# Kernel optimization log

Hardware: AMD Instinct MI355X
Metric: run time of the kernel (lower is better)

Reference implementation:

```python
import jax, jax.numpy as jnp
import numpy as np

EPS = 1e-5
BT_BATCH = 32       # BarlowTwinsLoss init batch_size (divides c)
BT_LAMBD = 0.005

def seg_sum(v, idx, n):
    return jax.ops.segment_sum(v, idx, num_segments=n)

def seg_mean(v, idx, n):
    s = seg_sum(v, idx, n)
    c = seg_sum(jnp.ones((v.shape[0],), v.dtype), idx, n)
    return s / jnp.maximum(c, 1.0)[:, None]

def gcn_conv(x, W, b, edge_index):
    n = x.shape[0]
    src, dst = edge_index[0], edge_index[1]
    xw = x @ W
    deg = 1.0 + seg_sum(jnp.ones(src.shape, x.dtype), dst, n)  # self-loop included
    norm = jax.lax.rsqrt(deg[src] * deg[dst])
    out = seg_sum(norm[:, None] * xw[src], dst, n) + xw / deg[:, None]
    return out + b

def barlow(z1, z2):
    # z-score with unbiased std (torch.std), then BatchNorm1d(affine=False) stats
    def std1(z):
        return (z - z.mean(0)) / jnp.std(z, axis=0, ddof=1)
    def bn(z):
        return (z - z.mean(0)) / jnp.sqrt(z.var(0) + EPS)
    a, b = bn(std1(z1)), bn(std1(z2))
    c = (a.T @ b) / BT_BATCH
    d = jnp.diagonal(c)
    on_diag = jnp.sum((d - 1.0) ** 2)
    off_diag = jnp.sum(c ** 2) - jnp.sum(d ** 2)
    return on_diag + BT_LAMBD * off_diag

def layernorm(t, g, b):
    m = t.mean(-1, keepdims=True)
    v = t.var(-1, keepdims=True)
    return g * (t - m) / jnp.sqrt(v + EPS) + b

def setup_inputs() -> dict:
    key = jax.random.key(0)
    ks = jax.random.split(key, 24)
    N, M, d, B = 50000, 10000, 128, 32
    NNZ, EG, EE = 200000, 600000, 160000
    s = 1.0 / np.sqrt(d)
    inp = {
        'x': jax.random.normal(ks[0], (N, d), jnp.float32),
        'hyperedge_feature': jax.random.normal(ks[1], (M, d), jnp.float32),
        'node_coord': jax.random.normal(ks[2], (N, 3), jnp.float32),
        'hyperedge_node_idx': jax.random.randint(ks[3], (NNZ,), 0, N),
        'hyperedge_edge_idx': jax.random.randint(ks[4], (NNZ,), 0, M),
        'node_batch_idx': jnp.sort(jax.random.randint(ks[5], (N,), 0, B)),
        'hyperedge_batch_idx': jnp.sort(jax.random.randint(ks[6], (M,), 0, B)),
        'X_X': jax.random.randint(ks[7], (2, EG), 0, N),
        'E_E': jax.random.randint(ks[8], (2, EE), 0, M),
        'num_graphs': B,
        'Wv': jax.random.normal(ks[9], (d, d), jnp.float32) * s,
        'bv': jnp.zeros((d,), jnp.float32),
        'We': jax.random.normal(ks[10], (d, d), jnp.float32) * s,
        'be': jnp.zeros((d,), jnp.float32),
        'Wx': jax.random.normal(ks[11], (d, d), jnp.float32) * s,
        'bx': jnp.zeros((d,), jnp.float32),
        'Weg': jax.random.normal(ks[12], (d, d), jnp.float32) * s,
        'beg': jnp.zeros((d,), jnp.float32),
        'ln_g': jnp.ones((d,), jnp.float32),
        'ln_b': jnp.zeros((d,), jnp.float32),
        'Wf': jax.random.normal(ks[13], (2 * d, d), jnp.float32) * (1.0 / np.sqrt(2 * d)),
        'bf': jnp.zeros((d,), jnp.float32),
    }
    return inp

def reference(x, hyperedge_feature, node_coord, hyperedge_node_idx, hyperedge_edge_idx,
              node_batch_idx, hyperedge_batch_idx, X_X, E_E, num_graphs,
              Wv, bv, We, be, Wx, bx, Weg, beg, ln_g, ln_b, Wf, bf):
    N, d = x.shape
    M = hyperedge_feature.shape[0]
    ni, ei = hyperedge_node_idx, hyperedge_edge_idx
    # E_HypergraphConv: node<->hyperedge bipartite message passing + EGNN-style coord update
    xw = x @ Wv + bv                     # [N, d]
    ew = hyperedge_feature @ We + be     # [M, d]
    e_conv = seg_mean(xw[ni], ei, M)     # hyperedge update from member nodes
    z_conv = seg_mean(ew[ei], ni, N)     # node update from incident hyperedges
    edge_coord = seg_mean(node_coord[ni], ei, M)          # [M, 3]
    rel = node_coord[ni] - edge_coord[ei]                 # [nnz, 3]
    phi = jnp.tanh(jnp.sum(xw[ni] * ew[ei], -1, keepdims=True)
                   * jax.lax.rsqrt(jnp.asarray(float(d), x.dtype)))
    update_coord = node_coord + seg_mean(rel * phi, ni, N)
    # implicit graph branches
    z_imp = gcn_conv(x, Wx, bx, X_X)
    e_imp = gcn_conv(hyperedge_feature, Weg, beg, E_E)
    bt_loss = barlow(z_imp, z_conv) + barlow(e_imp, e_conv)
    # norm -> GELU (erf, torch default) -> dropout(eval=identity) -> residual
    z = jax.nn.gelu(layernorm(z_conv, ln_g, ln_b), approximate=False) + x
    e = jax.nn.gelu(layernorm(e_conv, ln_g, ln_b), approximate=False) + hyperedge_feature
    z_graph = seg_mean(z, node_batch_idx, num_graphs)
    e_graph = seg_mean(e, hyperedge_batch_idx, num_graphs)
    graph = jnp.concatenate([z_graph, e_graph], axis=1) @ Wf + bf
    return z, e, update_coord, graph, bt_loss
```

## Files before the change

### kernel.cpp

```cpp
#include <hip/hip_runtime.h>
#include <hip/hip_bf16.h>

#define NB 32
#define GPN 448
#define GPM 80
#define RGRP 16

__device__ __forceinline__ float wave_sum(float v) {
#pragma unroll
  for (int off = 32; off; off >>= 1) v += __shfl_xor(v, off);
  return v;
}
__device__ __forceinline__ int wave_sum_i(int v) {
#pragma unroll
  for (int off = 32; off; off >>= 1) v += __shfl_xor(v, off);
  return v;
}

__device__ __forceinline__ float bf2f(unsigned short u) {
  return __uint_as_float(((unsigned int)u) << 16);
}
__device__ __forceinline__ unsigned short f2bf(float f) {
  unsigned int v = __float_as_uint(f);
  return (unsigned short)((v + 0x7FFFu + ((v >> 16) & 1u)) >> 16);
}

__device__ __forceinline__ void gemm_body(const float* __restrict__ X,
                                          const float* __restrict__ W1,
                                          const float* __restrict__ b1,
                                          unsigned short* __restrict__ out1,
                                          const float* __restrict__ W2,
                                          unsigned short* __restrict__ out2, int rows,
                                          int blk, unsigned short (*xs)[132]) {
  const int t = threadIdx.x;
  const int c4 = t & 31;
  const int rg = t >> 5;
  const int r0 = blk * 64;
#pragma unroll
  for (int i = 0; i < 8; i++) {
    const int idx = t + i * 256;
    const int row = idx >> 5, cc = idx & 31;
    const int gr = r0 + row;
    float4 v = make_float4(0.f, 0.f, 0.f, 0.f);
    if (gr < rows) v = ((const float4*)X)[(size_t)gr * 32 + cc];
    ushort4 u;
    u.x = f2bf(v.x); u.y = f2bf(v.y); u.z = f2bf(v.z); u.w = f2bf(v.w);
    *(ushort4*)&xs[row][cc * 4] = u;
  }
  __syncthreads();
  const float4* W1v = (const float4*)W1;
  const float4* W2v = (const float4*)W2;
  const float4 b4 = ((const float4*)b1)[c4];
  float4 acc1[8], acc2[8];
#pragma unroll
  for (int i = 0; i < 8; i++) {
    acc1[i] = b4;
    acc2[i] = make_float4(0.f, 0.f, 0.f, 0.f);
  }
  const int rbase = rg * 8;
#pragma unroll 2
  for (int k = 0; k < 128; k++) {
    const float4 w1 = W1v[k * 32 + c4];
    const float4 w2 = W2v[k * 32 + c4];
#pragma unroll
    for (int i = 0; i < 8; i++) {
      const float xv = bf2f(xs[rbase + i][k]);
      acc1[i].x = fmaf(xv, w1.x, acc1[i].x);
      acc1[i].y = fmaf(xv, w1.y, acc1[i].y);
      acc1[i].z = fmaf(xv, w1.z, acc1[i].z);
      acc1[i].w = fmaf(xv, w1.w, acc1[i].w);
      acc2[i].x = fmaf(xv, w2.x, acc2[i].x);
      acc2[i].y = fmaf(xv, w2.y, acc2[i].y);
      acc2[i].z = fmaf(xv, w2.z, acc2[i].z);
      acc2[i].w = fmaf(xv, w2.w, acc2[i].w);
    }
  }
#pragma unroll
  for (int i = 0; i < 8; i++) {
    const int gr = r0 + rbase + i;
    if (gr < rows) {
      ushort4 o1, o2;
      o1.x = f2bf(acc1[i].x); o1.y = f2bf(acc1[i].y);
      o1.z = f2bf(acc1[i].z); o1.w = f2bf(acc1[i].w);
      o2.x = f2bf(acc2[i].x); o2.y = f2bf(acc2[i].y);
      o2.z = f2bf(acc2[i].z); o2.w = f2bf(acc2[i].w);
      ((ushort4*)out1)[(size_t)gr * 32 + c4] = o1;
      ((ushort4*)out2)[(size_t)gr * 32 + c4] = o2;
    }
  }
}

__global__ __launch_bounds__(256) void fused_stage1(
    const float* __restrict__ x, const float* __restrict__ Wv,
    const float* __restrict__ bv, unsigned short* __restrict__ xw,
    const float* __restrict__ Wx, unsigned short* __restrict__ xw2, int N, int nbGN,
    const float* __restrict__ hf, const float* __restrict__ We,
    const float* __restrict__ be, unsigned short* __restrict__ ew,
    const float* __restrict__ Weg, unsigned short* __restrict__ ew2, int M, int nbG,
    int nbCnt, int mn, const int* __restrict__ ni, const int* __restrict__ ei,
    int nnz, const int* __restrict__ xx, int eg, const int* __restrict__ ee, int eeN,
    int* cnt_n, int* cnt_e, int* cnt_gx, int* cnt_ge, int* rank_pn, int* rank_pe,
    int* rank_g, int* rank_h, const float* __restrict__ coord, float* ec) {
  __shared__ unsigned short xs[64][132];
  const int b = blockIdx.x;
  int type, idx;
  const int mn2 = 2 * mn;
  if (b < mn2) {
    type = b & 1;
    idx = b >> 1;
  } else {
    type = (nbG > nbCnt) ? 0 : 1;
    idx = mn + (b - mn2);
  }
  if (type == 0) {
    if (idx < nbGN)
      gemm_body(x, Wv, bv, xw, Wx, xw2, N, idx, xs);
    else
      gemm_body(hf, We, be, ew, Weg, ew2, M, idx - nbGN, xs);
    return;
  }
  int i = idx * 1024 + (int)threadIdx.x;
#pragma unroll
  for (int k = 0; k < 4; k++, i += 256) {
    if (i < nnz) {
      const int n = ni[i], e = ei[i];
      rank_pn[i] = atomicAdd(&cnt_n[n], 1);
      rank_pe[i] = atomicAdd(&cnt_e[e], 1);
      atomicAdd(&ec[e * 3 + 0], coord[n * 3 + 0]);
      atomicAdd(&ec[e * 3 + 1], coord[n * 3 + 1]);
      atomicAdd(&ec[e * 3 + 2], coord[n * 3 + 2]);
    } else if (i < nnz + eg) {
      const int j = i - nnz;
      rank_g[j] = atomicAdd(&cnt_gx[xx[eg + j]], 1);
    } else if (i < nnz + eg + eeN) {
      const int j = i - nnz - eg;
      rank_h[j] = atomicAdd(&cnt_ge[ee[eeN + j]], 1);
    }
  }
}

__global__ __launch_bounds__(256) void scan_partial(
    const int* __restrict__ c0, int n0, const int* __restrict__ c1, int n1,
    const int* __restrict__ c2, int n2, const int* __restrict__ c3, int n3,
    int nb0, int nb1, int nb2, int nb3, int* __restrict__ bsums) {
  const int gb = blockIdx.x;
  const int* cnt;
  int lb, n;
  if (gb < nb0) { cnt = c0; lb = gb; n = n0; }
  else if (gb < nb0 + nb1) { cnt = c1; lb = gb - nb0; n = n1; }
  else if (gb < nb0 + nb1 + nb2) { cnt = c2; lb = gb - nb0 - nb1; n = n2; }
  else { cnt = c3; lb = gb - nb0 - nb1 - nb2; n = n3; }
  const int t = threadIdx.x;
  const int base = lb * 4096 + t * 16;
  int s = 0;
#pragma unroll
  for (int i = 0; i < 16; i++) {
    const int idx = base + i;
    if (idx < n) s += cnt[idx];
  }
  const int wsum = wave_sum_i(s);
  __shared__ int wsm[4];
  if ((t & 63) == 0) wsm[t >> 6] = wsum;
  __syncthreads();
  if (t == 0) bsums[gb] = wsm[0] + wsm[1] + wsm[2] + wsm[3];
}

__global__ void scan_bsums(const int* __restrict__ bsums, int nb0, int nb1, int nb2,
                           int nb3, int* __restrict__ bbase, int* __restrict__ totals) {
  if (threadIdx.x) return;
  int segs[4] = {nb0, nb1, nb2, nb3};
  int gb = 0;
  for (int a = 0; a < 4; a++) {
    int run = 0;
    for (int i = 0; i < segs[a]; i++) {
      bbase[gb] = run;
      run += bsums[gb];
      gb++;
    }
    totals[a] = run;
  }
}

__global__ __launch_bounds__(256) void scan_final(
    int* __restrict__ c0, int* rp0, float* rs0, float* ecd0, int n0,
    int* __restrict__ c1, int* rp1, float* rs1, float* ecd1, int n1,
    int* __restrict__ c2, int* rp2, float* rs2, float* ecd2, int n2,
    int* __restrict__ c3, int* rp3, float* rs3, float* ecd3, int n3,
    int nb0, int nb1, int nb2, int nb3, const int* __restrict__ bbase,
    const int* __restrict__ totals) {
  const int gb = blockIdx.x;
  int* cnt;
  int* rp;
  float* rs;
  float* ecd;
  int lb, n, a;
  if (gb < nb0) { cnt = c0; rp = rp0; rs = rs0; ecd = ecd0; lb = gb; n = n0; a = 0; }
  else if (gb < nb0 + nb1) { cnt = c1; rp = rp1; rs = rs1; ecd = ecd1; lb = gb - nb0; n = n1; a = 1; }
  else if (gb < nb0 + nb1 + nb2) { cnt = c2; rp = rp2; rs = rs2; ecd = ecd2; lb = gb - nb0 - nb1; n = n2; a = 2; }
  else { cnt = c3; rp = rp3; rs = rs3; ecd = ecd3; lb = gb - nb0 - nb1 - nb2; n = n3; a = 3; }
  const int t = threadIdx.x;
  const int base = lb * 4096 + t * 16;
  int vals[16];
  int s = 0;
#pragma unroll
  for (int i = 0; i < 16; i++) {
    const int idx = base + i;
    vals[i] = (idx < n) ? cnt[idx] : 0;
    s += vals[i];
  }
  __shared__ int tsum[256];
  tsum[t] = s;
  __syncthreads();
  for (int off = 1; off < 256; off <<= 1) {
    const int v = (t >= off) ? tsum[t - off] : 0;
    __syncthreads();
    tsum[t] += v;
    __syncthreads();
  }
  int run = bbase[gb] + (t ? tsum[t - 1] : 0);
#pragma unroll
  for (int i = 0; i < 16; i++) {
    const int idx = base + i;
    if (idx < n) {
      rp[idx] = run;
      if (rs) rs[idx] = rsqrtf(1.f + (float)vals[i]);
      if (ecd) {
        const float inv = 1.f / fmaxf((float)vals[i], 1.f);
        ecd[idx * 3 + 0] *= inv;
        ecd[idx * 3 + 1] *= inv;
        ecd[idx * 3 + 2] *= inv;
      }
      run += vals[i];
    }
  }
  if (t == 0 && lb == 0) rp[n] = totals[a];
}

__global__ __launch_bounds__(256) void fused_fill(
    const int* __restrict__ ni, const int* __restrict__ ei, int nnz,
    const int* __restrict__ xx, int eg, const int* __restrict__ ee, int eeN,
    const int* __restrict__ rp_n, const int* __restrict__ rp_e,
    const int* __restrict__ rp_gx, const int* __restrict__ rp_ge,
    const int* __restrict__ rank_pn, const int* __restrict__ rank_pe,
    const int* __restrict__ rank_g, const int* __restrict__ rank_h, int* adj_n,
    int* adj_e, int* adj_gx, int* adj_ge, int nbFill, const int* __restrict__ nbi,
    int n, int* cbn, const int* __restrict__ hbi, int m, int* cbe) {
  const int b = blockIdx.x;
  const int t = threadIdx.x;
  if (b < nbFill) {
    int i = b * 1024 + t;
#pragma unroll
    for (int k = 0; k < 4; k++, i += 256) {
      if (i < nnz) {
        const int n0 = ni[i], e0 = ei[i];
        adj_n[rp_n[n0] + rank_pn[i]] = e0;
        adj_e[rp_e[e0] + rank_pe[i]] = n0;
      } else if (i < nnz + eg) {
        const int j = i - nnz;
        adj_gx[rp_gx[xx[eg + j]] + rank_g[j]] = xx[j];
      } else if (i < nnz + eg + eeN) {
        const int j = i - nnz - eg;
        adj_ge[rp_ge[ee[eeN + j]] + rank_h[j]] = ee[j];
      }
    }
    return;
  }
  const bool B = (b - nbFill) != 0;
  const int* idx = B ? hbi : nbi;
  const int nn = B ? m : n;
  int* out = B ? cbe : cbn;
  const int g = t;
  if (g >= NB) return;
  int lo = 0, hi = nn;
  while (lo < hi) { int mid = (lo + hi) >> 1; if (idx[mid] < g) lo = mid + 1; else hi = mid; }
  const int l = lo;
  lo = 0; hi = nn;
  while (lo < hi) { int mid = (lo + hi) >> 1; if (idx[mid] < g + 1) lo = mid + 1; else hi = mid; }
  out[g] = lo - l;
}

__device__ __forceinline__ void gcn_body(const unsigned short* __restrict__ xw,
                                         const int* __restrict__ rowptr,
                                         const int* __restrict__ adj,
                                         const float* __restrict__ rs,
                                         const float* __restrict__ bias,
                                         float* __restrict__ out, int n, int lb) {
  const int r = (lb * 256 + (int)threadIdx.x) >> 6;
  const int lane = threadIdx.x & 63;
  if (r >= n) return;
  const int lo = rowptr[r], hi = rowptr[r + 1];
  const float rd = rs[r];
  float2 acc = make_float2(0.f, 0.f);
  for (int base = lo; base < hi; base += 64) {
    const int mm = min(64, hi - base);
    int aj = 0;
    float rj = 0.f;
    if (base + lane < hi) {
      aj = adj[base + lane];
      rj = rs[aj];
    }
    for (int j = 0; j < mm; j++) {
      const int s = __shfl(aj, j);
      const float w = __shfl(rj, j);
      const ushort2 u = ((const ushort2*)xw)[(size_t)s * 64 + lane];
      acc.x = fmaf(w, bf2f(u.x), acc.x);
      acc.y = fmaf(w, bf2f(u.y), acc.y);
    }
  }
  const ushort2 su = ((const ushort2*)xw)[(size_t)r * 64 + lane];
  const float2 bb = ((const float2*)bias)[lane];
  float2 o;
  o.x = fmaf(rd, acc.x, fmaf(rd * rd, bf2f(su.x), bb.x));
  o.y = fmaf(rd, acc.y, fmaf(rd * rd, bf2f(su.y), bb.y));
  ((float2*)out)[(size_t)r * 64 + lane] = o;
}

__global__ __launch_bounds__(256) void fused_gathers(
    const unsigned short* __restrict__ ew, const unsigned short* __restrict__ xw,
    const float* __restrict__ coord, const float* __restrict__ ecoord,
    const int* __restrict__ rp_n, const int* __restrict__ adj_n,
    float* __restrict__ z_conv, float* __restrict__ outc, int N, int nbNode,
    const unsigned short* __restrict__ xw2, const int* __restrict__ rp_gx,
    const int* __restrict__ adj_gx, const float* __restrict__ rs_gx,
    const float* __restrict__ bx, float* __restrict__ outz, int nbGcnN,
    const unsigned short* __restrict__ ew2, const int* __restrict__ rp_ge,
    const int* __restrict__ adj_ge, const float* __restrict__ rs_ge,
    const float* __restrict__ beg, float* __restrict__ oute, int M, int nbGcnM,
    const int* __restrict__ rp_e, const int* __restrict__ adj_e,
    float* __restrict__ e_conv) {
  const int b = blockIdx.x;
  const int t = threadIdx.x;
  const int lane = t & 63;
  if (b < nbNode) {
    const int r = (b * 256 + t) >> 6;
    if (r >= N) return;
    const int lo = rp_n[r], hi = rp_n[r + 1];
    const ushort2 au = ((const ushort2*)xw)[(size_t)r * 64 + lane];
    const float2 a = make_float2(bf2f(au.x), bf2f(au.y));
    const float myc = (lane < 3) ? coord[r * 3 + lane] : 0.f;
    float2 acc = make_float2(0.f, 0.f);
    float cacc = 0.f;
    for (int base = lo; base < hi; base += 64) {
      const int mm = min(64, hi - base);
      int aj = (base + lane < hi) ? adj_n[base + lane] : 0;
      for (int j = 0; j < mm; j++) {
        const int e = __shfl(aj, j);
        const ushort2 bu = ((const ushort2*)ew)[(size_t)e * 64 + lane];
        const float2 bb = make_float2(bf2f(bu.x), bf2f(bu.y));
        acc.x += bb.x;
        acc.y += bb.y;
        const float dot = wave_sum(fmaf(a.x, bb.x, a.y * bb.y));
        const float ph = tanhf(dot * 0.08838834764831845f);
        if (lane < 3) cacc = fmaf(myc - ecoord[e * 3 + lane], ph, cacc);
      }
    }
    const float inv = 1.f / fmaxf((float)(hi - lo), 1.f);
    ((float2*)z_conv)[(size_t)r * 64 + lane] = make_float2(acc.x * inv, acc.y * inv);
    if (lane < 3) outc[r * 3 + lane] = myc + cacc * inv;
    return;
  }
  if (b < nbNode + nbGcnN) {
    gcn_body(xw2, rp_gx, adj_gx, rs_gx, bx, outz, N, b - nbNode);
    return;
  }
  if (b < nbNode + nbGcnN + nbGcnM) {
    gcn_body(ew2, rp_ge, adj_ge, rs_ge, beg, oute, M, b - nbNode - nbGcnN);
    return;
  }
  const int lb = b - nbNode - nbGcnN - nbGcnM;
  const int e = (lb * 256 + t) >> 6;
  if (e >= M) return;
  const int lo = rp_e[e], hi = rp_e[e + 1];
  float2 acc = make_float2(0.f, 0.f);
  for (int base = lo; base < hi; base += 64) {
    const int mm = min(64, hi - base);
    int aj = (base + lane < hi) ? adj_e[base + lane] : 0;
    for (int j = 0; j < mm; j++) {
      const int nidx = __shfl(aj, j);
      const ushort2 vu = ((const ushort2*)xw)[(size_t)nidx * 64 + lane];
      acc.x += bf2f(vu.x);
      acc.y += bf2f(vu.y);
    }
  }
  const float inv = 1.f / fmaxf((float)(hi - lo), 1.f);
  ((float2*)e_conv)[(size_t)e * 64 + lane] = make_float2(acc.x * inv, acc.y * inv);
}

__global__ __launch_bounds__(256) void gram_partial2(
    const float* __restrict__ Z1a, const float* __restrict__ Z2a, int na,
    float* __restrict__ parta, const float* __restrict__ Z1b,
    const float* __restrict__ Z2b, int nbm, float* __restrict__ partb,
    float* __restrict__ st, int nblkA) {
  const bool A = (int)blockIdx.x < nblkA;
  const int pid = A ? blockIdx.x : blockIdx.x - nblkA;
  const float* Z1 = A ? Z1a : Z1b;
  const float* Z2 = A ? Z2a : Z2b;
  const int n = A ? na : nbm;
  const int gparts = A ? GPN : GPM;
  float* part = (A ? parta : partb) + (size_t)pid * 16384;
  float* sum1 = st + (A ? 0 : 512);
  float* ssq1 = sum1 + 128;
  float* sum2 = sum1 + 256;
  float* ssq2 = sum1 + 384;
  __shared__ float4 s1[256], s2[256];
  const int t = threadIdx.x;
  const int ti = t >> 4, tj = t & 15;
  const int rpb = (n + gparts - 1) / gparts;
  const int lo = pid * rpb, hi = min(lo + rpb, n);
  float acc[8][8];
#pragma unroll
  for (int i = 0; i < 8; i++)
#pragma unroll
    for (int j = 0; j < 8; j++) acc[i][j] = 0.f;
  float cs = 0.f, cq = 0.f;
  const float* s1f = (const float*)s1;
  const float* s2f = (const float*)s2;
  const int c = t & 127;
  const bool low = t < 128;
  for (int rb = lo; rb < hi; rb += 8) {
    const int nr = min(8, hi - rb);
    __syncthreads();
    if (t < nr * 32) {
      const int rr = rb + (t >> 5);
      s1[t] = ((const float4*)Z1)[(size_t)rr * 32 + (t & 31)];
      s2[t] = ((const float4*)Z2)[(size_t)rr * 32 + (t & 31)];
    }
    __syncthreads();
    for (int r = 0; r < nr; r++) {
      const float4 a0 = s1[r * 32 + ti * 2], a1 = s1[r * 32 + ti * 2 + 1];
      const float4 b0 = s2[r * 32 + tj * 2], b1 = s2[r * 32 + tj * 2 + 1];
      const float av[8] = {a0.x, a0.y, a0.z, a0.w, a1.x, a1.y, a1.z, a1.w};
      const float bv[8] = {b0.x, b0.y, b0.z, b0.w, b1.x, b1.y, b1.z, b1.w};
#pragma unroll
      for (int i = 0; i < 8; i++)
#pragma unroll
        for (int j = 0; j < 8; j++) acc[i][j] = fmaf(av[i], bv[j], acc[i][j]);
      const float v = low ? s1f[r * 128 + c] : s2f[r * 128 + c];
      cs += v;
      cq = fmaf(v, v, cq);
    }
  }
  float4* P = (float4*)part;
#pragma unroll
  for (int i = 0; i < 8; i++) {
    P[(ti * 8 + i) * 32 + tj * 2] = make_float4(acc[i][0], acc[i][1], acc[i][2], acc[i][3]);
    P[(ti * 8 + i) * 32 + tj * 2 + 1] = make_float4(acc[i][4], acc[i][5], acc[i][6], acc[i][7]);
  }
  if (low) {
    atomicAdd(&sum1[c], cs);
    atomicAdd(&ssq1[c], cq);
  } else {
    atomicAdd(&sum2[c], cs);
    atomicAdd(&ssq2[c], cq);
  }
}

__global__ __launch_bounds__(256) void fused_reduce_ln(
    const float* __restrict__ parta, float* __restrict__ G1,
    const float* __restrict__ partb, float* __restrict__ G2,
    const float* __restrict__ convA, const float* __restrict__ residA,
    float* __restrict__ outA, int nA, int lnA, const float* __restrict__ convB,
    const float* __restrict__ residB, float* __restrict__ outB, int nBm,
    const float* __restrict__ g, const float* __restrict__ bvec) {
  const int b = blockIdx.x;
  const int t = threadIdx.x;
  const int NRED = (GPN / RGRP + GPM / RGRP) * 16;
  if (b < NRED) {
    const int nga = GPN / RGRP;
    const int slice = b & 15;
    const int grp = b >> 4;
    const bool A = grp < nga;
    const float* part = A ? parta : partb;
    float* G = A ? G1 : G2;
    const int g0 = (A ? grp : grp - nga) * RGRP;
    const int e = slice * 1024 + t * 4;
    float4 s = make_float4(0.f, 0.f, 0.f, 0.f);
#pragma unroll 4
    for (int p = 0; p < RGRP; p++) {
      const float4 v = *(const float4*)&part[(size_t)(g0 + p) * 16384 + e];
      s.x += v.x;
      s.y += v.y;
      s.z += v.z;
      s.w += v.w;
    }
    atomicAdd(&G[e], s.x);
    atomicAdd(&G[e + 1], s.y);
    atomicAdd(&G[e + 2], s.z);
    atomicAdd(&G[e + 3], s.w);
    return;
  }
  const int b2 = b - NRED;
  const bool A = b2 < lnA;
  const int lb = A ? b2 : b2 - lnA;
  const float* conv = A ? convA : convB;
  const float* resid = A ? residA : residB;
  float* out = A ? outA : outB;
  const int rows = A ? nA : nBm;
  const int w = (lb * 256 + t) >> 6;
  const int lane = t & 63;
  if (w >= rows) return;
  const float2 v = ((const float2*)conv)[(size_t)w * 64 + lane];
  const float m = wave_sum(v.x + v.y) * (1.f / 128.f);
  const float q = wave_sum(fmaf(v.x, v.x, v.y * v.y)) * (1.f / 128.f);
  const float rstd = rsqrtf(q - m * m + 1e-5f);
  const float2 gg = ((const float2*)g)[lane];
  const float2 bb = ((const float2*)bvec)[lane];
  const float2 rr = ((const float2*)resid)[(size_t)w * 64 + lane];
  float y0 = fmaf(gg.x, (v.x - m) * rstd, bb.x);
  float y1 = fmaf(gg.y, (v.y - m) * rstd, bb.y);
  y0 = 0.5f * y0 * (1.f + erff(y0 * 0.7071067811865476f));
  y1 = 0.5f * y1 * (1.f + erff(y1 * 0.7071067811865476f));
  float2 o;
  o.x = y0 + rr.x;
  o.y = y1 + rr.y;
  ((float2*)out)[(size_t)w * 64 + lane] = o;
}

__global__ __launch_bounds__(256) void fused_fin_pool(
    const float* __restrict__ G1, const float* __restrict__ G2,
    const float* __restrict__ st, float nA, float nB, float* outbt,
    const float* __restrict__ ZA, const int* __restrict__ bidxA, int n, int spA,
    float* poolA, const float* __restrict__ ZB, const int* __restrict__ bidxB, int m,
    float* poolB) {
  __shared__ float s1s[128], m1s[128], s2s[128], m2s[128];
  __shared__ float red[256];
  const int b = blockIdx.x;
  const int t = threadIdx.x;
  if (b < 2) {
    const bool A = b == 0;
    const float* G = A ? G1 : G2;
    const float* sum1 = st + (A ? 0 : 512);
    const float* ssq1 = sum1 + 128;
    const float* sum2 = sum1 + 256;
    const float* ssq2 = sum1 + 384;
    const float nn = A ? nA : nB;
    if (t < 128) {
      const float inv_n = 1.f / nn;
      const float bnf = (nn - 1.f) * inv_n + 1e-5f;
      float mu = sum1[t] * inv_n;
      float vu = (ssq1[t] * inv_n - mu * mu) * nn / (nn - 1.f);
      s1s[t] = rsqrtf(vu * bnf);
      m1s[t] = mu;
      mu = sum2[t] * inv_n;
      vu = (ssq2[t] * inv_n - mu * mu) * nn / (nn - 1.f);
      s2s[t] = rsqrtf(vu * bnf);
      m2s[t] = mu;
    }
    __syncthreads();
    float on = 0.f, off = 0.f;
    for (int idx = t; idx < 16384; idx += 256) {
      const int i = idx >> 7, j = idx & 127;
      const float c = s1s[i] * s2s[j] * (G[idx] - nn * m1s[i] * m2s[j]) * (1.f / 32.f);
      if (i == j) {
        const float dd = c - 1.f;
        on += dd * dd;
      } else {
        off += c * c;
      }
    }
    red[t] = on + 0.005f * off;
    __syncthreads();
    for (int s = 128; s; s >>= 1) {
      if (t < s) red[t] += red[t + s];
      __syncthreads();
    }
    if (t == 0) atomicAdd(outbt, red[0]);
    return;
  }
  const int pb = b - 2;
  const bool A = pb < spA;
  const int lb = A ? pb : pb - spA;
  const float* Z = A ? ZA : ZB;
  const int* bidx = A ? bidxA : bidxB;
  const int n2 = A ? n : m;
  float* pool = A ? poolA : poolB;
  const int c = t & 127;
  const int h = t >> 7;
  const int r0 = lb * 128 + h * 64;
  const int re = min(lb * 128 + (h + 1) * 64, n2);
  if (r0 >= n2) return;
  float acc = 0.f;
  int cur = bidx[r0];
  for (int r = r0; r < re; r++) {
    const int bb = bidx[r];
    if (bb != cur) {
      atomicAdd(&pool[cur * 128 + c], acc);
      acc = 0.f;
      cur = bb;
    }
    acc += Z[(size_t)r * 128 + c];
  }
  atomicAdd(&pool[cur * 128 + c], acc);
}

__global__ __launch_bounds__(128) void graph_gemm(
    const float* __restrict__ zg, const float* __restrict__ eg,
    const int* __restrict__ cnz, const int* __restrict__ cne,
    const float* __restrict__ Wf, const float* __restrict__ bf, float* out) {
  __shared__ float cat[256];
  const int g = blockIdx.x, t = threadIdx.x;
  cat[t] = zg[g * 128 + t] / fmaxf((float)cnz[g], 1.f);
  cat[128 + t] = eg[g * 128 + t] / fmaxf((float)cne[g], 1.f);
  __syncthreads();
  float acc = bf[t];
#pragma unroll 8
  for (int k = 0; k < 256; k++) acc = fmaf(cat[k], Wf[k * 128 + t], acc);
  out[g * 128 + t] = acc;
}

extern "C" void kernel_launch(void* const* d_in, const int* in_sizes, int n_in,
                              void* d_out, int out_size, void* d_ws, size_t ws_size,
                              hipStream_t stream) {
  const float* x = (const float*)d_in[0];
  const float* hf = (const float*)d_in[1];
  const float* coord = (const float*)d_in[2];
  const int* ni = (const int*)d_in[3];
  const int* ei = (const int*)d_in[4];
  const int* nb = (const int*)d_in[5];
  const int* hb = (const int*)d_in[6];
  const int* xx = (const int*)d_in[7];
  const int* ee = (const int*)d_in[8];
  const float* Wv = (const float*)d_in[10];
  const float* bv = (const float*)d_in[11];
  const float* We = (const float*)d_in[12];
  const float* be = (const float*)d_in[13];
  const float* Wx = (const float*)d_in[14];
  const float* bx = (const float*)d_in[15];
  const float* Weg = (const float*)d_in[16];
  const float* beg = (const float*)d_in[17];
  const float* lng = (const float*)d_in[18];
  const float* lnb = (const float*)d_in[19];
  const float* Wf = (const float*)d_in[20];
  const float* bf = (const float*)d_in[21];

  const int N = in_sizes[0] / 128;
  const int M = in_sizes[1] / 128;
  const int NNZ = in_sizes[3];
  const int EG = in_sizes[7] / 2;
  const int EE = in_sizes[8] / 2;

  float* ws = (float*)d_ws;
  size_t o = 0;
  unsigned short* xw = (unsigned short*)(ws + o);  o += (size_t)N * 64;
  unsigned short* ew = (unsigned short*)(ws + o);  o += (size_t)M * 64;
  unsigned short* xw2 = (unsigned short*)(ws + o); o += (size_t)N * 64;
  unsigned short* ew2 = (unsigned short*)(ws + o); o += (size_t)M * 64;
  int* rank_pn = (int*)(ws + o); o += NNZ;
  int* rank_pe = (int*)(ws + o); o += NNZ;
  int* rank_g = (int*)(ws + o);  o += EG;
  int* rank_h = (int*)(ws + o);  o += EE;
  float* z_conv = ws + o; o += (size_t)N * 128;
  float* e_conv = ws + o; o += (size_t)M * 128;
  float* rs_gx = ws + o;  o += N;
  float* rs_ge = ws + o;  o += M;
  const size_t fz0 = o;
  float* ecoord = ws + o; o += (size_t)M * 3;
  float* G1 = ws + o;     o += 16384;
  float* G2 = ws + o;     o += 16384;
  float* st = ws + o;     o += 1024;
  float* zg = ws + o;     o += NB * 128;
  float* eg_p = ws + o;   o += NB * 128;
  const size_t fz1 = o;
  int* wsi = (int*)(ws + o);
  size_t oi = 0;
  int* cnt_n = wsi + oi;  oi += N;
  int* cnt_e = wsi + oi;  oi += M;
  int* cnt_gx = wsi + oi; oi += N;
  int* cnt_ge = wsi + oi; oi += M;
  const size_t iz1 = oi;
  int* rp_n = wsi + oi;   oi += N + 1;
  int* rp_e = wsi + oi;   oi += M + 1;
  int* rp_gx = wsi + oi;  oi += N + 1;
  int* rp_ge = wsi + oi;  oi += M + 1;
  int* adj_n = wsi + oi;  oi += NNZ;
  int* adj_e = wsi + oi;  oi += NNZ;
  int* adj_gx = wsi + oi; oi += EG;
  int* adj_ge = wsi + oi; oi += EE;
  int* cbn = wsi + oi;    oi += NB;
  int* cbe = wsi + oi;    oi += NB;
  int* bsums = wsi + oi;  oi += 64;
  int* bbase = wsi + oi;  oi += 64;
  int* totals = wsi + oi; oi += 4;

  float* gpartA = ws;
  float* gpartB = ws + (size_t)GPN * 16384;

  float* outz = (float*)d_out;
  float* oute = outz + (size_t)N * 128;
  float* outc = oute + (size_t)M * 128;
  float* outg = outc + (size_t)N * 3;
  float* outbt = outg + NB * 128;

  hipMemsetAsync(ws + fz0, 0, (fz1 - fz0) * 4, stream);
  hipMemsetAsync(wsi, 0, iz1 * 4, stream);
  hipMemsetAsync(outbt, 0, 4, stream);

  const int nbGN = (N + 63) / 64, nbGM = (M + 63) / 64;
  const int nbG = nbGN + nbGM;
  const int tot = NNZ + EG + EE;
  const int nbCnt = (tot + 1023) >> 10;
  const int mn = (nbG < nbCnt) ? nbG : nbCnt;
  fused_stage1<<<nbG + nbCnt, 256, 0, stream>>>(
      x, Wv, bv, xw, Wx, xw2, N, nbGN, hf, We, be, ew, Weg, ew2, M, nbG, nbCnt, mn,
      ni, ei, NNZ, xx, EG, ee, EE, cnt_n, cnt_e, cnt_gx, cnt_ge, rank_pn, rank_pe,
      rank_g, rank_h, coord, ecoord);

  const int nb0 = (N + 4095) >> 12, nb1 = (M + 4095) >> 12;
  const int sgrid = 2 * nb0 + 2 * nb1;
  scan_partial<<<sgrid, 256, 0, stream>>>(cnt_n, N, cnt_e, M, cnt_gx, N, cnt_ge, M,
                                          nb0, nb1, nb0, nb1, bsums);
  scan_bsums<<<1, 64, 0, stream>>>(bsums, nb0, nb1, nb0, nb1, bbase, totals);
  scan_final<<<sgrid, 256, 0, stream>>>(
      cnt_n, rp_n, nullptr, nullptr, N, cnt_e, rp_e, nullptr, ecoord, M, cnt_gx,
      rp_gx, rs_gx, nullptr, N, cnt_ge, rp_ge, rs_ge, nullptr, M, nb0, nb1, nb0, nb1,
      bbase, totals);

  const int nbFill = (tot + 1023) >> 10;
  fused_fill<<<nbFill + 2, 256, 0, stream>>>(
      ni, ei, NNZ, xx, EG, ee, EE, rp_n, rp_e, rp_gx, rp_ge, rank_pn, rank_pe, rank_g,
      rank_h, adj_n, adj_e, adj_gx, adj_ge, nbFill, nb, N, cbn, hb, M, cbe);

  const int nbNode = (N + 3) / 4, nbGcnN = (N + 3) / 4, nbGcnM = (M + 3) / 4,
            nbHedge = (M + 3) / 4;
  fused_gathers<<<nbNode + nbGcnN + nbGcnM + nbHedge, 256, 0, stream>>>(
      ew, xw, coord, ecoord, rp_n, adj_n, z_conv, outc, N, nbNode, xw2, rp_gx, adj_gx,
      rs_gx, bx, outz, nbGcnN, ew2, rp_ge, adj_ge, rs_ge, beg, oute, M, nbGcnM, rp_e,
      adj_e, e_conv);

  gram_partial2<<<GPN + GPM, 256, 0, stream>>>(outz, z_conv, N, gpartA, oute, e_conv,
                                               M, gpartB, st, GPN);

  const int lnA = (N + 3) / 4;
  fused_reduce_ln<<<(GPN / RGRP + GPM / RGRP) * 16 + lnA + (M + 3) / 4, 256, 0,
                    stream>>>(gpartA, G1, gpartB, G2, z_conv, x, outz, N, lnA, e_conv,
                              hf, oute, M, lng, lnb);

  const int spA = (N + 127) / 128, spB = (M + 127) / 128;
  fused_fin_pool<<<2 + spA + spB, 256, 0, stream>>>(G1, G2, st, (float)N, (float)M,
                                                    outbt, outz, nb, N, spA, zg, oute,
                                                    hb, M, eg_p);

  graph_gemm<<<NB, 128, 0, stream>>>(zg, eg_p, cbn, cbe, Wf, bf, outg);
}
```

Measured before the change: 370.3 us.

## Move dense GEMM blocks from count kernel into CSR fill kernel

The node and hyperedge projection GEMM blocks move out of the first kernel, which interleaved them with the atomic counting blocks. Counting now runs alone in its own kernel, and the GEMM blocks launch together with the CSR fill blocks after the scans. The aim is to shorten the atomic-heavy counting phase so it reaches the scan sooner, and to overlap the GEMM with the fill scatter instead. The risk is that the GEMM work simply lands on a different critical segment, and the fill kernel now needs GEMM shared memory for every block.

```diff
diff --git a/kernel.cpp b/kernel.cpp
--- a/kernel.cpp
+++ b/kernel.cpp
@@ -25,101 +25,13 @@
   return (unsigned short)((v + 0x7FFFu + ((v >> 16) & 1u)) >> 16);
 }
 
-__device__ __forceinline__ void gemm_body(const float* __restrict__ X,
-                                          const float* __restrict__ W1,
-                                          const float* __restrict__ b1,
-                                          unsigned short* __restrict__ out1,
-                                          const float* __restrict__ W2,
-                                          unsigned short* __restrict__ out2, int rows,
-                                          int blk, unsigned short (*xs)[132]) {
-  const int t = threadIdx.x;
-  const int c4 = t & 31;
-  const int rg = t >> 5;
-  const int r0 = blk * 64;
-#pragma unroll
-  for (int i = 0; i < 8; i++) {
-    const int idx = t + i * 256;
-    const int row = idx >> 5, cc = idx & 31;
-    const int gr = r0 + row;
-    float4 v = make_float4(0.f, 0.f, 0.f, 0.f);
-    if (gr < rows) v = ((const float4*)X)[(size_t)gr * 32 + cc];
-    ushort4 u;
-    u.x = f2bf(v.x); u.y = f2bf(v.y); u.z = f2bf(v.z); u.w = f2bf(v.w);
-    *(ushort4*)&xs[row][cc * 4] = u;
-  }
-  __syncthreads();
-  const float4* W1v = (const float4*)W1;
-  const float4* W2v = (const float4*)W2;
-  const float4 b4 = ((const float4*)b1)[c4];
-  float4 acc1[8], acc2[8];
-#pragma unroll
-  for (int i = 0; i < 8; i++) {
-    acc1[i] = b4;
-    acc2[i] = make_float4(0.f, 0.f, 0.f, 0.f);
-  }
-  const int rbase = rg * 8;
-#pragma unroll 2
-  for (int k = 0; k < 128; k++) {
-    const float4 w1 = W1v[k * 32 + c4];
-    const float4 w2 = W2v[k * 32 + c4];
-#pragma unroll
-    for (int i = 0; i < 8; i++) {
-      const float xv = bf2f(xs[rbase + i][k]);
-      acc1[i].x = fmaf(xv, w1.x, acc1[i].x);
-      acc1[i].y = fmaf(xv, w1.y, acc1[i].y);
-      acc1[i].z = fmaf(xv, w1.z, acc1[i].z);
-      acc1[i].w = fmaf(xv, w1.w, acc1[i].w);
-      acc2[i].x = fmaf(xv, w2.x, acc2[i].x);
-      acc2[i].y = fmaf(xv, w2.y, acc2[i].y);
-      acc2[i].z = fmaf(xv, w2.z, acc2[i].z);
-      acc2[i].w = fmaf(xv, w2.w, acc2[i].w);
-    }
-  }
-#pragma unroll
-  for (int i = 0; i < 8; i++) {
-    const int gr = r0 + rbase + i;
-    if (gr < rows) {
-      ushort4 o1, o2;
-      o1.x = f2bf(acc1[i].x); o1.y = f2bf(acc1[i].y);
-      o1.z = f2bf(acc1[i].z); o1.w = f2bf(acc1[i].w);
-      o2.x = f2bf(acc2[i].x); o2.y = f2bf(acc2[i].y);
-      o2.z = f2bf(acc2[i].z); o2.w = f2bf(acc2[i].w);
-      ((ushort4*)out1)[(size_t)gr * 32 + c4] = o1;
-      ((ushort4*)out2)[(size_t)gr * 32 + c4] = o2;
-    }
-  }
-}
-
-__global__ __launch_bounds__(256) void fused_stage1(
-    const float* __restrict__ x, const float* __restrict__ Wv,
-    const float* __restrict__ bv, unsigned short* __restrict__ xw,
-    const float* __restrict__ Wx, unsigned short* __restrict__ xw2, int N, int nbGN,
-    const float* __restrict__ hf, const float* __restrict__ We,
-    const float* __restrict__ be, unsigned short* __restrict__ ew,
-    const float* __restrict__ Weg, unsigned short* __restrict__ ew2, int M, int nbG,
-    int nbCnt, int mn, const int* __restrict__ ni, const int* __restrict__ ei,
-    int nnz, const int* __restrict__ xx, int eg, const int* __restrict__ ee, int eeN,
-    int* cnt_n, int* cnt_e, int* cnt_gx, int* cnt_ge, int* rank_pn, int* rank_pe,
-    int* rank_g, int* rank_h, const float* __restrict__ coord, float* ec) {
-  __shared__ unsigned short xs[64][132];
-  const int b = blockIdx.x;
-  int type, idx;
-  const int mn2 = 2 * mn;
-  if (b < mn2) {
-    type = b & 1;
-    idx = b >> 1;
-  } else {
-    type = (nbG > nbCnt) ? 0 : 1;
-    idx = mn + (b - mn2);
-  }
-  if (type == 0) {
-    if (idx < nbGN)
-      gemm_body(x, Wv, bv, xw, Wx, xw2, N, idx, xs);
-    else
-      gemm_body(hf, We, be, ew, Weg, ew2, M, idx - nbGN, xs);
-    return;
-  }
-  int i = idx * 1024 + (int)threadIdx.x;
+__global__ void count_kernel(const int* __restrict__ ni, const int* __restrict__ ei,
+                             int nnz, const int* __restrict__ xx, int eg,
+                             const int* __restrict__ ee, int eeN, int* cnt_n,
+                             int* cnt_e, int* cnt_gx, int* cnt_ge, int* rank_pn,
+                             int* rank_pe, int* rank_g, int* rank_h,
+                             const float* __restrict__ coord, float* ec) {
+  int i = blockIdx.x * 1024 + (int)threadIdx.x;
 #pragma unroll
   for (int k = 0; k < 4; k++, i += 256) {
     if (i < nnz) {
@@ -135,6 +47,71 @@
     } else if (i < nnz + eg + eeN) {
       const int j = i - nnz - eg;
       rank_h[j] = atomicAdd(&cnt_ge[ee[eeN + j]], 1);
+    }
+  }
+}
+
+__device__ __forceinline__ void gemm_body(const float* __restrict__ X,
+                                          const float* __restrict__ W1,
+                                          const float* __restrict__ b1,
+                                          unsigned short* __restrict__ out1,
+                                          const float* __restrict__ W2,
+                                          unsigned short* __restrict__ out2, int rows,
+                                          int blk, unsigned short (*xs)[132]) {
+  const int t = threadIdx.x;
+  const int c4 = t & 31;
+  const int rg = t >> 5;
+  const int r0 = blk * 64;
+#pragma unroll
+  for (int i = 0; i < 8; i++) {
+    const int idx = t + i * 256;
+    const int row = idx >> 5, cc = idx & 31;
+    const int gr = r0 + row;
+    float4 v = make_float4(0.f, 0.f, 0.f, 0.f);
+    if (gr < rows) v = ((const float4*)X)[(size_t)gr * 32 + cc];
+    ushort4 u;
+    u.x = f2bf(v.x); u.y = f2bf(v.y); u.z = f2bf(v.z); u.w = f2bf(v.w);
+    *(ushort4*)&xs[row][cc * 4] = u;
+  }
+  __syncthreads();
+  const float4* W1v = (const float4*)W1;
+  const float4* W2v = (const float4*)W2;
+  const float4 b4 = ((const float4*)b1)[c4];
+  float4 acc1[8], acc2[8];
+#pragma unroll
+  for (int i = 0; i < 8; i++) {
+    acc1[i] = b4;
+    acc2[i] = make_float4(0.f, 0.f, 0.f, 0.f);
+  }
+  const int rbase = rg * 8;
+#pragma unroll 2
+  for (int k = 0; k < 128; k++) {
+    const float4 w1 = W1v[k * 32 + c4];
+    const float4 w2 = W2v[k * 32 + c4];
+#pragma unroll
+    for (int i = 0; i < 8; i++) {
+      const float xv = bf2f(xs[rbase + i][k]);
+      acc1[i].x = fmaf(xv, w1.x, acc1[i].x);
+      acc1[i].y = fmaf(xv, w1.y, acc1[i].y);
+      acc1[i].z = fmaf(xv, w1.z, acc1[i].z);
+      acc1[i].w = fmaf(xv, w1.w, acc1[i].w);
+      acc2[i].x = fmaf(xv, w2.x, acc2[i].x);
+      acc2[i].y = fmaf(xv, w2.y, acc2[i].y);
+      acc2[i].z = fmaf(xv, w2.z, acc2[i].z);
+      acc2[i].w = fmaf(xv, w2.w, acc2[i].w);
+    }
+  }
+#pragma unroll
+  for (int i = 0; i < 8; i++) {
+    const int gr = r0 + rbase + i;
+    if (gr < rows) {
+      ushort4 o1, o2;
+      o1.x = f2bf(acc1[i].x); o1.y = f2bf(acc1[i].y);
+      o1.z = f2bf(acc1[i].z); o1.w = f2bf(acc1[i].w);
+      o2.x = f2bf(acc2[i].x); o2.y = f2bf(acc2[i].y);
+      o2.z = f2bf(acc2[i].z); o2.w = f2bf(acc2[i].w);
+      ((ushort4*)out1)[(size_t)gr * 32 + c4] = o1;
+      ((ushort4*)out2)[(size_t)gr * 32 + c4] = o2;
     }
   }
 }
@@ -236,7 +213,13 @@
   if (t == 0 && lb == 0) rp[n] = totals[a];
 }
 
-__global__ __launch_bounds__(256) void fused_fill(
+__global__ __launch_bounds__(256) void fused_fill_gemm(
+    const float* __restrict__ x, const float* __restrict__ Wv,
+    const float* __restrict__ bv, unsigned short* __restrict__ xw,
+    const float* __restrict__ Wx, unsigned short* __restrict__ xw2, int N, int nbGN,
+    const float* __restrict__ hf, const float* __restrict__ We,
+    const float* __restrict__ be, unsigned short* __restrict__ ew,
+    const float* __restrict__ Weg, unsigned short* __restrict__ ew2, int M, int nbG,
     const int* __restrict__ ni, const int* __restrict__ ei, int nnz,
     const int* __restrict__ xx, int eg, const int* __restrict__ ee, int eeN,
     const int* __restrict__ rp_n, const int* __restrict__ rp_e,
@@ -244,11 +227,20 @@
     const int* __restrict__ rank_pn, const int* __restrict__ rank_pe,
     const int* __restrict__ rank_g, const int* __restrict__ rank_h, int* adj_n,
     int* adj_e, int* adj_gx, int* adj_ge, int nbFill, const int* __restrict__ nbi,
-    int n, int* cbn, const int* __restrict__ hbi, int m, int* cbe) {
+    int* cbn, const int* __restrict__ hbi, int* cbe) {
+  __shared__ unsigned short xs[64][132];
   const int b = blockIdx.x;
   const int t = threadIdx.x;
-  if (b < nbFill) {
-    int i = b * 1024 + t;
+  if (b < nbG) {
+    if (b < nbGN)
+      gemm_body(x, Wv, bv, xw, Wx, xw2, N, b, xs);
+    else
+      gemm_body(hf, We, be, ew, Weg, ew2, M, b - nbGN, xs);
+    return;
+  }
+  const int fb = b - nbG;
+  if (fb < nbFill) {
+    int i = fb * 1024 + t;
 #pragma unroll
     for (int k = 0; k < 4; k++, i += 256) {
       if (i < nnz) {
@@ -265,9 +257,9 @@
     }
     return;
   }
-  const bool B = (b - nbFill) != 0;
+  const bool B = (fb - nbFill) != 0;
   const int* idx = B ? hbi : nbi;
-  const int nn = B ? m : n;
+  const int nn = B ? M : N;
   int* out = B ? cbe : cbn;
   const int g = t;
   if (g >= NB) return;
@@ -695,15 +687,11 @@
   hipMemsetAsync(wsi, 0, iz1 * 4, stream);
   hipMemsetAsync(outbt, 0, 4, stream);
 
-  const int nbGN = (N + 63) / 64, nbGM = (M + 63) / 64;
-  const int nbG = nbGN + nbGM;
   const int tot = NNZ + EG + EE;
   const int nbCnt = (tot + 1023) >> 10;
-  const int mn = (nbG < nbCnt) ? nbG : nbCnt;
-  fused_stage1<<<nbG + nbCnt, 256, 0, stream>>>(
-      x, Wv, bv, xw, Wx, xw2, N, nbGN, hf, We, be, ew, Weg, ew2, M, nbG, nbCnt, mn,
-      ni, ei, NNZ, xx, EG, ee, EE, cnt_n, cnt_e, cnt_gx, cnt_ge, rank_pn, rank_pe,
-      rank_g, rank_h, coord, ecoord);
+  count_kernel<<<nbCnt, 256, 0, stream>>>(ni, ei, NNZ, xx, EG, ee, EE, cnt_n, cnt_e,
+                                          cnt_gx, cnt_ge, rank_pn, rank_pe, rank_g,
+                                          rank_h, coord, ecoord);
 
   const int nb0 = (N + 4095) >> 12, nb1 = (M + 4095) >> 12;
   const int sgrid = 2 * nb0 + 2 * nb1;
@@ -715,10 +703,13 @@
       rp_gx, rs_gx, nullptr, N, cnt_ge, rp_ge, rs_ge, nullptr, M, nb0, nb1, nb0, nb1,
       bbase, totals);
 
+  const int nbGN = (N + 63) / 64, nbGM = (M + 63) / 64;
+  const int nbG = nbGN + nbGM;
   const int nbFill = (tot + 1023) >> 10;
-  fused_fill<<<nbFill + 2, 256, 0, stream>>>(
-      ni, ei, NNZ, xx, EG, ee, EE, rp_n, rp_e, rp_gx, rp_ge, rank_pn, rank_pe, rank_g,
-      rank_h, adj_n, adj_e, adj_gx, adj_ge, nbFill, nb, N, cbn, hb, M, cbe);
+  fused_fill_gemm<<<nbG + nbFill + 2, 256, 0, stream>>>(
+      x, Wv, bv, xw, Wx, xw2, N, nbGN, hf, We, be, ew, Weg, ew2, M, nbG, ni, ei, NNZ,
+      xx, EG, ee, EE, rp_n, rp_e, rp_gx, rp_ge, rank_pn, rank_pe, rank_g, rank_h,
+      adj_n, adj_e, adj_gx, adj_ge, nbFill, nb, cbn, hb, cbe);
 
   const int nbNode = (N + 3) / 4, nbGcnN = (N + 3) / 4, nbGcnM = (M + 3) / 4,
             nbHedge = (M + 3) / 4;
```

Measured after the change: 387.8 us. +4.7%, slower.
